# Kernel optimization log

Measured on AMD Instinct MI355X. Metric: run time of the kernel, lower is better.

Reference implementation:

```python
import jax, jax.numpy as jnp
import numpy as np

N, E, D, G, L = 100_000, 500_000, 128, 512, 4
BN_EPS = 1e-5

def _bn(v, g, b):
    # BatchNorm1d in training mode: biased batch stats over node/graph axis
    m = v.mean(0)
    var = v.var(0)
    return (v - m) * jax.lax.rsqrt(var + BN_EPS) * g + b

def setup_inputs() -> dict:
    key = jax.random.key(0)
    ks = jax.random.split(key, 12)
    s = 0.05
    return {
        "x": jax.random.normal(ks[0], (N, D), jnp.float32),
        "edge_index": jax.random.randint(ks[1], (2, E), 0, N, jnp.int64),
        "batch": jnp.sort(jax.random.randint(ks[2], (N,), 0, G, jnp.int64)),
        "num_graphs": G,
        "W1": jax.random.normal(ks[3], (L, D, 2 * D), jnp.float32) * s,
        "b1": jnp.zeros((L, 2 * D), jnp.float32),
        "g1": jnp.ones((L, 2 * D), jnp.float32),
        "be1": jnp.zeros((L, 2 * D), jnp.float32),
        "W2": jax.random.normal(ks[4], (L, 2 * D, D), jnp.float32) * s,
        "b2": jnp.zeros((L, D), jnp.float32),
        "gbn": jnp.ones((L, D), jnp.float32),
        "bbn": jnp.zeros((L, D), jnp.float32),
        "eps": jnp.zeros((L,), jnp.float32),
        "cW1": jax.random.normal(ks[5], (3 * D, D), jnp.float32) * s,
        "cb1": jnp.zeros((D,), jnp.float32),
        "cg": jnp.ones((D,), jnp.float32),
        "cbeta": jnp.zeros((D,), jnp.float32),
        "cW2": jax.random.normal(ks[6], (D, D // 2), jnp.float32) * s,
        "cb2": jnp.zeros((D // 2,), jnp.float32),
        "cW3": jax.random.normal(ks[7], (D // 2, 2), jnp.float32) * s,
        "cb3": jnp.zeros((2,), jnp.float32),
    }

def reference(x, edge_index, batch, num_graphs, W1, b1, g1, be1, W2, b2, gbn, bbn, eps,
              cW1, cb1, cg, cbeta, cW2, cb2, cW3, cb3):
    n = x.shape[0]
    src, dst = edge_index[0], edge_index[1]
    for l in range(W1.shape[0]):
        # GINConv: mlp((1+eps)*x + sum_{j in N(i)} x_j)  (scatter-add to dst)
        agg = jax.ops.segment_sum(x[src], dst, num_segments=n)
        h = (1.0 + eps[l]) * x + agg
        h = jax.nn.relu(_bn(h @ W1[l] + b1[l], g1[l], be1[l]))
        h = h @ W2[l] + b2[l]
        x = jax.nn.relu(_bn(h, gbn[l], bbn[l]))  # outer BN + ReLU (dropout off: eval)
    # multi-pool readout: add / mean / max per graph
    s = jax.ops.segment_sum(x, batch, num_segments=num_graphs)
    cnt = jax.ops.segment_sum(jnp.ones((n,), x.dtype), batch, num_segments=num_graphs)
    mean = s / jnp.maximum(cnt, 1.0)[:, None]
    mx = jax.ops.segment_max(x, batch, num_segments=num_graphs)
    z = jnp.concatenate([s, mean, mx], axis=-1)  # [G, 3*D]
    z = jax.nn.relu(_bn(z @ cW1 + cb1, cg, cbeta))
    z = jax.nn.relu(z @ cW2 + cb2)
    return z @ cW3 + cb3
```

## Files before the change

kernel.cpp:

```cpp
#include <hip/hip_runtime.h>
#include <cstdint>
#include <cstddef>

#define NN 100000
#define EE 500000
#define DD 128
#define GG 512
#define LL 4
#define BN_EPS 1e-5f

typedef __attribute__((ext_vector_type(8))) short short8;
typedef __attribute__((ext_vector_type(8))) unsigned short ushort8v;
typedef __attribute__((ext_vector_type(4))) float f32x4;

static __device__ __forceinline__ unsigned short f2bf(float f) {
  union { float f; unsigned u; } v;
  v.f = f;
  unsigned r = v.u + 0x7fffu + ((v.u >> 16) & 1u);
  return (unsigned short)(r >> 16);
}
static __device__ __forceinline__ float bf2f(unsigned short u) {
  union { unsigned u; float f; } v;
  v.u = ((unsigned)u) << 16;
  return v.f;
}


__global__ void k_hist(const int* __restrict__ ei, int* __restrict__ cnt) {
  int e = blockIdx.x * 256 + threadIdx.x;
  if (e < EE) {
    int d = ei[EE + e];
    if (d >= 0 && d < NN) atomicAdd(&cnt[d], 1);
  }
}

__global__ void k_part(const int* __restrict__ cnt, int* __restrict__ part) {
  __shared__ int sm[1024];
  int t = threadIdx.x;
  int i = blockIdx.x * 1024 + t;
  sm[t] = (i < NN) ? cnt[i] : 0;
  __syncthreads();
  for (int off = 512; off > 0; off >>= 1) {
    if (t < off) sm[t] += sm[t + off];
    __syncthreads();
  }
  if (t == 0) part[blockIdx.x] = sm[0];
}

__global__ void k_scanpart(const int* __restrict__ part, int* __restrict__ partx, int nb) {
  __shared__ int sm[128];
  int t = threadIdx.x;
  int v = (t < nb) ? part[t] : 0;
  sm[t] = v;
  __syncthreads();
  for (int off = 1; off < 128; off <<= 1) {
    int u = (t >= off) ? sm[t - off] : 0;
    __syncthreads();
    sm[t] += u;
    __syncthreads();
  }
  if (t < nb) partx[t] = sm[t] - v;
}

__global__ void k_rs(const int* __restrict__ cnt, const int* __restrict__ partx,
                     int* __restrict__ rs, int* __restrict__ cur) {
  __shared__ int sm[1024];
  int t = threadIdx.x;
  int i = blockIdx.x * 1024 + t;
  int v = (i < NN) ? cnt[i] : 0;
  sm[t] = v;
  __syncthreads();
  for (int off = 1; off < 1024; off <<= 1) {
    int u = (t >= off) ? sm[t - off] : 0;
    __syncthreads();
    sm[t] += u;
    __syncthreads();
  }
  if (i < NN) {
    int excl = partx[blockIdx.x] + sm[t] - v;
    rs[i] = excl;
    cur[i] = excl;
    if (i == NN - 1) rs[NN] = excl + v;
  }
}

__global__ void k_fill(const int* __restrict__ ei, int* __restrict__ cur,
                       int* __restrict__ ci) {
  int e = blockIdx.x * 256 + threadIdx.x;
  if (e < EE) {
    int s = ei[e];
    int d = ei[EE + e];
    if (d >= 0 && d < NN && s >= 0 && s < NN) {
      int pos = atomicAdd(&cur[d], 1);
      if (pos >= 0 && pos < EE) ci[pos] = s;
    }
  }
}


__global__ void k_conv(const float* __restrict__ W1, const float* __restrict__ W2,
                       unsigned short* __restrict__ W1t, unsigned short* __restrict__ W2t) {
  int idx = blockIdx.x * 256 + threadIdx.x;
  if (idx < 4 * 256 * 128) {
    {
      int l = idx >> 15, rem = idx & 32767;
      int nc = rem >> 7, k = rem & 127;
      W1t[idx] = f2bf(W1[(l << 15) + k * 256 + nc]);
    }
    {
      int l = idx >> 15, rem = idx & 32767;
      int nc = rem >> 8, k = rem & 255;
      W2t[idx] = f2bf(W2[(l << 15) + k * 128 + nc]);
    }
  }
}


__global__ void k_x2bf(const float* __restrict__ x, unsigned short* __restrict__ xb) {
  int i = blockIdx.x * 256 + threadIdx.x;
  if (i < NN * DD / 4) {
    float4 v = *(const float4*)(x + (size_t)i * 4);
    ushort4 o;
    o.x = f2bf(v.x); o.y = f2bf(v.y); o.z = f2bf(v.z); o.w = f2bf(v.w);
    *(ushort4*)(xb + (size_t)i * 4) = o;
  }
}


__global__ __launch_bounds__(256) void k_agg_bf16(
    const unsigned short* __restrict__ X, const int* __restrict__ rs,
    const int* __restrict__ ci, const float* __restrict__ epsv, int l, int mode,
    const float* __restrict__ tsc, const float* __restrict__ tsh,
    unsigned short* __restrict__ h0, int n) {
  int idx = blockIdx.x * 256 + threadIdx.x;
  int node = idx >> 4;
  int c8 = (idx & 15) << 3;
  if (node >= n) return;
  float sa[8], sb[8];
  if (mode) {
    float4 a0 = *(const float4*)(tsc + c8), a1 = *(const float4*)(tsc + c8 + 4);
    float4 b0 = *(const float4*)(tsh + c8), b1 = *(const float4*)(tsh + c8 + 4);
    sa[0] = a0.x; sa[1] = a0.y; sa[2] = a0.z; sa[3] = a0.w;
    sa[4] = a1.x; sa[5] = a1.y; sa[6] = a1.z; sa[7] = a1.w;
    sb[0] = b0.x; sb[1] = b0.y; sb[2] = b0.z; sb[3] = b0.w;
    sb[4] = b1.x; sb[5] = b1.y; sb[6] = b1.z; sb[7] = b1.w;
  }
  float se = 1.f + epsv[l];
  ushort8v v = *(const ushort8v*)(X + (size_t)node * DD + c8);
  float acc[8];
#pragma unroll
  for (int j = 0; j < 8; ++j) {
    float f = bf2f(v[j]);
    if (mode) f = fmaxf(0.f, f * sa[j] + sb[j]);
    acc[j] = se * f;
  }
  int e0 = rs[node], e1 = rs[node + 1];
  ushort8v un;
  if (e0 < e1) un = *(const ushort8v*)(X + (size_t)ci[e0] * DD + c8);
  for (int e = e0; e < e1; ++e) {
    ushort8v uc = un;
    if (e + 1 < e1) un = *(const ushort8v*)(X + (size_t)ci[e + 1] * DD + c8);
#pragma unroll
    for (int j = 0; j < 8; ++j) {
      float f = bf2f(uc[j]);
      if (mode) f = fmaxf(0.f, f * sa[j] + sb[j]);
      acc[j] += f;
    }
  }
  ushort8v o;
#pragma unroll
  for (int j = 0; j < 8; ++j) o[j] = f2bf(acc[j]);
  *(ushort8v*)(h0 + (size_t)node * DD + c8) = o;
}


template <int K, int NC>
__global__ __launch_bounds__(512) void k_gemm(
    const unsigned short* __restrict__ A, int mode, const float* __restrict__ tsc,
    const float* __restrict__ tsh, const unsigned short* __restrict__ Bt,
    const float* __restrict__ bias, unsigned short* __restrict__ C,
    float* __restrict__ psum, float* __restrict__ psq, int n) {
  constexpr int KC = 64;
  constexpr int KT = K / KC;
  constexpr int NT = NC / 128;
  constexpr int P = KT * NT;
  constexpr int AST = 72;
  constexpr int CTP = 136;
  __shared__ __align__(16) unsigned short smem[2 * 128 * AST];
  __shared__ float bsum[128], bsq[128];
  unsigned short* Asm = smem;
  unsigned short* Bsm = smem + 128 * AST;
  unsigned short* Ct = smem;

  int tid = threadIdx.x;
  int lane = tid & 63, wave = tid >> 6;
  int quad = lane >> 4, l15 = lane & 15;
  int row0 = blockIdx.x * 128;
  int blk = blockIdx.x;

  ushort8v pa[2], pb[2];
#pragma unroll
  for (int it = 0; it < 2; ++it) {
    int f = tid + it * 512;
    int r = f >> 3;
    int c8 = (f & 7) << 3;
    int gr = row0 + r;
    pa[it] = (ushort8v){0, 0, 0, 0, 0, 0, 0, 0};
    if (gr < n) pa[it] = *(const ushort8v*)(A + (size_t)gr * K + c8);
    pb[it] = *(const ushort8v*)(Bt + (size_t)r * K + c8);
  }

  f32x4 acc[8];
  for (int p = 0; p < P; ++p) {
    int cg = p / KT, kc = p % KT;
    if (kc == 0) {
#pragma unroll
      for (int j = 0; j < 8; ++j) acc[j] = (f32x4){0.f, 0.f, 0.f, 0.f};
    }
#pragma unroll
    for (int it = 0; it < 2; ++it) {
      int f = tid + it * 512;
      int r = f >> 3;
      int c8 = (f & 7) << 3;
      ushort8v v = pa[it];
      if (mode) {
        int kg = kc * KC + c8;
        float4 s0 = *(const float4*)(tsc + kg);
        float4 s1 = *(const float4*)(tsc + kg + 4);
        float4 t0 = *(const float4*)(tsh + kg);
        float4 t1 = *(const float4*)(tsh + kg + 4);
        float sa[8] = {s0.x, s0.y, s0.z, s0.w, s1.x, s1.y, s1.z, s1.w};
        float sb[8] = {t0.x, t0.y, t0.z, t0.w, t1.x, t1.y, t1.z, t1.w};
#pragma unroll
        for (int j = 0; j < 8; ++j)
          v[j] = f2bf(fmaxf(0.f, bf2f(v[j]) * sa[j] + sb[j]));
      }
      *(ushort8v*)(&Asm[r * AST + c8]) = v;
      *(ushort8v*)(&Bsm[r * AST + c8]) = pb[it];
    }
    __syncthreads();
    if (p + 1 < P) {
      int cg2 = (p + 1) / KT, kc2 = (p + 1) % KT;
#pragma unroll
      for (int it = 0; it < 2; ++it) {
        int f = tid + it * 512;
        int r = f >> 3;
        int c8 = (f & 7) << 3;
        int gr = row0 + r;
        pa[it] = (ushort8v){0, 0, 0, 0, 0, 0, 0, 0};
        if (gr < n) pa[it] = *(const ushort8v*)(A + (size_t)gr * K + kc2 * KC + c8);
        pb[it] = *(const ushort8v*)(Bt + (size_t)(cg2 * 128 + r) * K + kc2 * KC + c8);
      }
    }
#pragma unroll
    for (int kk = 0; kk < KC; kk += 32) {
      int ko = kk + quad * 8;
      short8 av = *(const short8*)(&Asm[(wave * 16 + l15) * AST + ko]);
#pragma unroll
      for (int cf = 0; cf < 8; ++cf) {
        short8 bv = *(const short8*)(&Bsm[(cf * 16 + l15) * AST + ko]);
        acc[cf] = __builtin_amdgcn_mfma_f32_16x16x32_bf16(av, bv, acc[cf], 0, 0, 0);
      }
    }
    if (kc == KT - 1) {
      __syncthreads();
      if (tid < 128) { bsum[tid] = 0.f; bsq[tid] = 0.f; }
      float s8[8], q8[8];
#pragma unroll
      for (int j = 0; j < 8; ++j) { s8[j] = 0.f; q8[j] = 0.f; }
      int lrbase = wave * 16 + quad * 4;
#pragma unroll
      for (int cf = 0; cf < 8; ++cf) {
        int col = cg * 128 + cf * 16 + l15;
        float bv = bias[col];
#pragma unroll
        for (int reg = 0; reg < 4; ++reg) {
          int lr = lrbase + reg;
          float e = acc[cf][reg] + bv;
          Ct[lr * CTP + cf * 16 + l15] = f2bf(e);
          if (row0 + lr < n) { s8[cf] += e; q8[cf] += e * e; }
        }
      }
#pragma unroll
      for (int cf = 0; cf < 8; ++cf) {
        s8[cf] += __shfl_xor(s8[cf], 16, 64);
        s8[cf] += __shfl_xor(s8[cf], 32, 64);
        q8[cf] += __shfl_xor(q8[cf], 16, 64);
        q8[cf] += __shfl_xor(q8[cf], 32, 64);
      }
      __syncthreads();
      if (quad == 0) {
#pragma unroll
        for (int cf = 0; cf < 8; ++cf) {
          atomicAdd(&bsum[cf * 16 + l15], s8[cf]);
          atomicAdd(&bsq[cf * 16 + l15], q8[cf]);
        }
      }
#pragma unroll
      for (int it = 0; it < 4; ++it) {
        int f = tid + it * 512;
        int r = f >> 4;
        int c8 = (f & 15) << 3;
        int gr = row0 + r;
        if (gr < n)
          *(ushort8v*)(C + (size_t)gr * NC + cg * 128 + c8) =
              *(const ushort8v*)(&Ct[r * CTP + c8]);
      }
      __syncthreads();
      if (tid < 128) {
        psum[(size_t)blk * NC + cg * 128 + tid] = bsum[tid];
        psq[(size_t)blk * NC + cg * 128 + tid] = bsq[tid];
      }
    } else {
      __syncthreads();
    }
  }
}


__global__ __launch_bounds__(256) void k_finred(
    const float* __restrict__ psum, const float* __restrict__ psq, int nb, int nc,
    const float* __restrict__ g, const float* __restrict__ be,
    float* __restrict__ osc, float* __restrict__ osh, float invn) {
  __shared__ float ws[4], wq[4];
  int col = blockIdx.x;
  int t = threadIdx.x;
  float s = 0.f, q = 0.f;
  for (int b = t; b < nb; b += 256) {
    s += psum[(size_t)b * nc + col];
    q += psq[(size_t)b * nc + col];
  }
#pragma unroll
  for (int off = 32; off > 0; off >>= 1) {
    s += __shfl_xor(s, off, 64);
    q += __shfl_xor(q, off, 64);
  }
  if ((t & 63) == 0) { ws[t >> 6] = s; wq[t >> 6] = q; }
  __syncthreads();
  if (t == 0) {
    s = ws[0] + ws[1] + ws[2] + ws[3];
    q = wq[0] + wq[1] + wq[2] + wq[3];
    float m = s * invn;
    float v = fmaxf(q * invn - m * m, 0.f);
    float sc = g[col] * rsqrtf(v + BN_EPS);
    osc[col] = sc;
    osh[col] = be[col] - m * sc;
  }
}


__global__ __launch_bounds__(256) void k_statz(
    const float* __restrict__ z1, const float* __restrict__ g,
    const float* __restrict__ be, float* __restrict__ osc, float* __restrict__ osh) {
  __shared__ float ws[4], wq[4];
  int col = blockIdx.x;
  int t = threadIdx.x;
  float s = 0.f, q = 0.f;
  for (int b = t; b < GG; b += 256) {
    float v = z1[(size_t)b * 128 + col];
    s += v;
    q += v * v;
  }
#pragma unroll
  for (int off = 32; off > 0; off >>= 1) {
    s += __shfl_xor(s, off, 64);
    q += __shfl_xor(q, off, 64);
  }
  if ((t & 63) == 0) { ws[t >> 6] = s; wq[t >> 6] = q; }
  __syncthreads();
  if (t == 0) {
    s = ws[0] + ws[1] + ws[2] + ws[3];
    q = wq[0] + wq[1] + wq[2] + wq[3];
    float m = s / (float)GG;
    float v = fmaxf(q / (float)GG - m * m, 0.f);
    float sc = g[col] * rsqrtf(v + BN_EPS);
    osc[col] = sc;
    osh[col] = be[col] - m * sc;
  }
}


static __device__ __forceinline__ int lb_i32(const int* a, int n, int key) {
  int lo = 0, hi = n;
  while (lo < hi) {
    int mid = (lo + hi) >> 1;
    if (a[mid] < key) lo = mid + 1; else hi = mid;
  }
  return lo;
}

__global__ __launch_bounds__(512) void k_pool(
    const unsigned short* __restrict__ X, const int* __restrict__ batch,
    const float* __restrict__ tsc, const float* __restrict__ tsh,
    float* __restrict__ z, int n) {
  __shared__ int slo, shi;
  __shared__ float ssum[8][128], smax[8][128];
  int g = blockIdx.x;
  int t = threadIdx.x;
  int sg = t >> 6;
  int c2 = (t & 63) << 1;
  if (t == 0) {
    slo = lb_i32(batch, n, g);
    shi = lb_i32(batch, n, g + 1);
  }
  __syncthreads();
  int lo = slo, hi = shi;
  float a0 = tsc[c2], a1 = tsc[c2 + 1];
  float b0 = tsh[c2], b1 = tsh[c2 + 1];
  float s0 = 0.f, s1 = 0.f;
  float m0 = -3.402823466e38f, m1 = -3.402823466e38f;
  for (int i = lo + sg; i < hi; i += 8) {
    unsigned u = *(const unsigned*)(X + (size_t)i * DD + c2);
    float v0 = fmaxf(0.f, bf2f((unsigned short)(u & 0xffff)) * a0 + b0);
    float v1 = fmaxf(0.f, bf2f((unsigned short)(u >> 16)) * a1 + b1);
    s0 += v0; m0 = fmaxf(m0, v0);
    s1 += v1; m1 = fmaxf(m1, v1);
  }
  ssum[sg][c2] = s0; ssum[sg][c2 + 1] = s1;
  smax[sg][c2] = m0; smax[sg][c2 + 1] = m1;
  __syncthreads();
  if (t < 128) {
    float S = 0.f, M = -3.402823466e38f;
#pragma unroll
    for (int k = 0; k < 8; ++k) {
      S += ssum[k][t];
      M = fmaxf(M, smax[k][t]);
    }
    float cntf = (float)(hi - lo);
    z[(size_t)g * 384 + t] = S;
    z[(size_t)g * 384 + 128 + t] = S / fmaxf(cntf, 1.f);
    z[(size_t)g * 384 + 256 + t] = M;
  }
}


__global__ void k_cls1(const float* __restrict__ z, const float* __restrict__ cW1,
                       const float* __restrict__ cb1, float* __restrict__ z1) {
  __shared__ float zr[384];
  int g = blockIdx.x;
  int c = threadIdx.x;
  for (int i = c; i < 384; i += 128) zr[i] = z[(size_t)g * 384 + i];
  __syncthreads();
  float s = cb1[c];
#pragma unroll 4
  for (int k = 0; k < 384; ++k) s = fmaf(zr[k], cW1[(size_t)k * 128 + c], s);
  z1[(size_t)g * 128 + c] = s;
}

__global__ void k_cls2(const float* __restrict__ z1, const float* __restrict__ csc,
                       const float* __restrict__ csh, const float* __restrict__ cW2,
                       const float* __restrict__ cb2, const float* __restrict__ cW3,
                       const float* __restrict__ cb3, float* __restrict__ out) {
  __shared__ float z1n[128];
  __shared__ float z2s[64];
  int g = blockIdx.x;
  int t = threadIdx.x;
  z1n[t] = fmaxf(0.f, z1[(size_t)g * 128 + t] * csc[t] + csh[t]);
  __syncthreads();
  if (t < 64) {
    float s = cb2[t];
#pragma unroll 4
    for (int k = 0; k < 128; ++k) s = fmaf(z1n[k], cW2[(size_t)k * 64 + t], s);
    z2s[t] = fmaxf(0.f, s);
  }
  __syncthreads();
  if (t < 2) {
    float s = cb3[t];
#pragma unroll 4
    for (int c = 0; c < 64; ++c) s = fmaf(z2s[c], cW3[(size_t)c * 2 + t], s);
    out[(size_t)g * 2 + t] = s;
  }
}


extern "C" void kernel_launch(void* const* d_in, const int* in_sizes, int n_in,
                              void* d_out, int out_size, void* d_ws, size_t ws_size,
                              hipStream_t stream) {
  const float* x = (const float*)d_in[0];
  const int* ei = (const int*)d_in[1];
  const int* batch = (const int*)d_in[2];
  const float* W1 = (const float*)d_in[4];
  const float* b1 = (const float*)d_in[5];
  const float* g1 = (const float*)d_in[6];
  const float* be1 = (const float*)d_in[7];
  const float* W2 = (const float*)d_in[8];
  const float* b2 = (const float*)d_in[9];
  const float* gbn = (const float*)d_in[10];
  const float* bbn = (const float*)d_in[11];
  const float* epsv = (const float*)d_in[12];
  const float* cW1 = (const float*)d_in[13];
  const float* cb1 = (const float*)d_in[14];
  const float* cg = (const float*)d_in[15];
  const float* cbeta = (const float*)d_in[16];
  const float* cW2 = (const float*)d_in[17];
  const float* cb2 = (const float*)d_in[18];
  const float* cW3 = (const float*)d_in[19];
  const float* cb3 = (const float*)d_in[20];
  float* out = (float*)d_out;

  char* p = (char*)d_ws;
  auto alloc = [&](size_t bytes) {
    char* r = p;
    p += (bytes + 255) & ~(size_t)255;
    return r;
  };
  const int NB = (NN + 127) / 128;
  int* cnt = (int*)alloc((size_t)NN * 4);
  int* rs = (int*)alloc((size_t)(NN + 1) * 4);
  int* cur = (int*)alloc((size_t)NN * 4);
  int* ci = (int*)alloc((size_t)EE * 4);
  int* part = (int*)alloc(128 * 4);
  int* partx = (int*)alloc(128 * 4);
  unsigned short* xbf = (unsigned short*)alloc((size_t)NN * DD * 2);
  unsigned short* h0 = (unsigned short*)alloc((size_t)NN * DD * 2);
  unsigned short* h1 = (unsigned short*)alloc((size_t)NN * 2 * DD * 2);
  unsigned short* xp = (unsigned short*)alloc((size_t)NN * DD * 2);
  float* psum = (float*)alloc((size_t)NB * 256 * 4);
  float* psq = (float*)alloc((size_t)NB * 256 * 4);
  float* tsc1 = (float*)alloc(256 * 4);
  float* tsh1 = (float*)alloc(256 * 4);
  float* tscX = (float*)alloc(128 * 4);
  float* tshX = (float*)alloc(128 * 4);
  float* zbuf = (float*)alloc((size_t)GG * 384 * 4);
  float* z1 = (float*)alloc((size_t)GG * 128 * 4);
  unsigned short* W1t = (unsigned short*)alloc((size_t)4 * 256 * 128 * 2);
  unsigned short* W2t = (unsigned short*)alloc((size_t)4 * 128 * 256 * 2);
  (void)ws_size; (void)n_in; (void)in_sizes; (void)out_size;

  k_conv<<<512, 256, 0, stream>>>(W1, W2, W1t, W2t);
  k_x2bf<<<(NN * DD / 4 + 255) / 256, 256, 0, stream>>>(x, xbf);

  hipMemsetAsync(cnt, 0, (size_t)NN * 4, stream);
  k_hist<<<(EE + 255) / 256, 256, 0, stream>>>(ei, cnt);
  const int nscan = (NN + 1023) / 1024;
  k_part<<<nscan, 1024, 0, stream>>>(cnt, part);
  k_scanpart<<<1, 128, 0, stream>>>(part, partx, nscan);
  k_rs<<<nscan, 1024, 0, stream>>>(cnt, partx, rs, cur);
  k_fill<<<(EE + 255) / 256, 256, 0, stream>>>(ei, cur, ci);

  for (int l = 0; l < LL; ++l) {
    const unsigned short* Xl = (l == 0) ? xbf : xp;
    k_agg_bf16<<<(NN * 16 + 255) / 256, 256, 0, stream>>>(
        Xl, rs, ci, epsv, l, (l > 0) ? 1 : 0, tscX, tshX, h0, NN);
    k_gemm<128, 256><<<NB, 512, 0, stream>>>(
        h0, 0, nullptr, nullptr, W1t + (size_t)l * 256 * 128,
        b1 + (size_t)l * 256, h1, psum, psq, NN);
    k_finred<<<256, 256, 0, stream>>>(psum, psq, NB, 256, g1 + (size_t)l * 256,
                                      be1 + (size_t)l * 256, tsc1, tsh1, 1.0f / NN);
    k_gemm<256, 128><<<NB, 512, 0, stream>>>(
        h1, 1, tsc1, tsh1, W2t + (size_t)l * 128 * 256,
        b2 + (size_t)l * 128, xp, psum, psq, NN);
    k_finred<<<128, 256, 0, stream>>>(psum, psq, NB, 128, gbn + (size_t)l * 128,
                                      bbn + (size_t)l * 128, tscX, tshX, 1.0f / NN);
  }

  k_pool<<<GG, 512, 0, stream>>>(xp, batch, tscX, tshX, zbuf, NN);
  k_cls1<<<GG, 128, 0, stream>>>(zbuf, cW1, cb1, z1);
  k_statz<<<128, 256, 0, stream>>>(z1, cg, cbeta, tscX, tshX);
  k_cls2<<<GG, 128, 0, stream>>>(z1, tscX, tshX, cW2, cb2, cW3, cb3, out);
}
```

Baseline: 765.7 us.

## Keep A fragments in registers and stage full weight matrix in LDS for GEMM

Rewrites the fused GEMM+BN-stats kernel so each wave loads its 16-row A slice straight into registers for the full K, stages the whole transposed weight matrix in LDS once, and computes all output columns in one pass with swapped MFMA operands. The per-K-chunk LDS staging of A and the associated barriers go away, and output is written directly from registers without an LDS transpose. Column statistics are reduced with lane shuffles plus a per-wave LDS buffer. In exchange it holds many accumulators and A registers (CF up to 16 f32x4, KT up to 8 short8), which raises register pressure, and the weight tile occupies a large LDS footprint (up to 256x136 shorts ≈ 68KB), while the launch bound now requests 4 blocks per CU.

```diff
diff --git a/kernel.cpp b/kernel.cpp
--- a/kernel.cpp
+++ b/kernel.cpp
@@ -175,145 +175,113 @@
 
 
 template <int K, int NC>
-__global__ __launch_bounds__(512) void k_gemm(
+__global__ __launch_bounds__(512, 4) void k_gemm(
     const unsigned short* __restrict__ A, int mode, const float* __restrict__ tsc,
     const float* __restrict__ tsh, const unsigned short* __restrict__ Bt,
     const float* __restrict__ bias, unsigned short* __restrict__ C,
     float* __restrict__ psum, float* __restrict__ psq, int n) {
-  constexpr int KC = 64;
-  constexpr int KT = K / KC;
-  constexpr int NT = NC / 128;
-  constexpr int P = KT * NT;
-  constexpr int AST = 72;
-  constexpr int CTP = 136;
-  __shared__ __align__(16) unsigned short smem[2 * 128 * AST];
-  __shared__ float bsum[128], bsq[128];
-  unsigned short* Asm = smem;
-  unsigned short* Bsm = smem + 128 * AST;
-  unsigned short* Ct = smem;
+  constexpr int KT = K / 32;
+  constexpr int CF = NC / 16;
+  constexpr int BP = K + 8;
+  constexpr int CH = K / 8;
+  __shared__ __align__(16) unsigned short Bsm[NC * BP];
 
   int tid = threadIdx.x;
   int lane = tid & 63, wave = tid >> 6;
   int quad = lane >> 4, l15 = lane & 15;
-  int row0 = blockIdx.x * 128;
-  int blk = blockIdx.x;
-
-  ushort8v pa[2], pb[2];
-#pragma unroll
-  for (int it = 0; it < 2; ++it) {
+  int r = blockIdx.x * 128 + wave * 16 + l15;
+  bool valid = r < n;
+
+  short8 av[KT];
+#pragma unroll
+  for (int ks = 0; ks < KT; ++ks) {
+    av[ks] = (short8){0, 0, 0, 0, 0, 0, 0, 0};
+    if (valid) av[ks] = *(const short8*)(A + (size_t)r * K + ks * 32 + quad * 8);
+  }
+
+#pragma unroll
+  for (int it = 0; it < NC * CH / 512; ++it) {
     int f = tid + it * 512;
-    int r = f >> 3;
-    int c8 = (f & 7) << 3;
-    int gr = row0 + r;
-    pa[it] = (ushort8v){0, 0, 0, 0, 0, 0, 0, 0};
-    if (gr < n) pa[it] = *(const ushort8v*)(A + (size_t)gr * K + c8);
-    pb[it] = *(const ushort8v*)(Bt + (size_t)r * K + c8);
-  }
-
-  f32x4 acc[8];
-  for (int p = 0; p < P; ++p) {
-    int cg = p / KT, kc = p % KT;
-    if (kc == 0) {
-#pragma unroll
-      for (int j = 0; j < 8; ++j) acc[j] = (f32x4){0.f, 0.f, 0.f, 0.f};
-    }
-#pragma unroll
-    for (int it = 0; it < 2; ++it) {
-      int f = tid + it * 512;
-      int r = f >> 3;
-      int c8 = (f & 7) << 3;
-      ushort8v v = pa[it];
-      if (mode) {
-        int kg = kc * KC + c8;
-        float4 s0 = *(const float4*)(tsc + kg);
-        float4 s1 = *(const float4*)(tsc + kg + 4);
-        float4 t0 = *(const float4*)(tsh + kg);
-        float4 t1 = *(const float4*)(tsh + kg + 4);
-        float sa[8] = {s0.x, s0.y, s0.z, s0.w, s1.x, s1.y, s1.z, s1.w};
-        float sb[8] = {t0.x, t0.y, t0.z, t0.w, t1.x, t1.y, t1.z, t1.w};
-#pragma unroll
-        for (int j = 0; j < 8; ++j)
-          v[j] = f2bf(fmaxf(0.f, bf2f(v[j]) * sa[j] + sb[j]));
-      }
-      *(ushort8v*)(&Asm[r * AST + c8]) = v;
-      *(ushort8v*)(&Bsm[r * AST + c8]) = pb[it];
-    }
-    __syncthreads();
-    if (p + 1 < P) {
-      int cg2 = (p + 1) / KT, kc2 = (p + 1) % KT;
-#pragma unroll
-      for (int it = 0; it < 2; ++it) {
-        int f = tid + it * 512;
-        int r = f >> 3;
-        int c8 = (f & 7) << 3;
-        int gr = row0 + r;
-        pa[it] = (ushort8v){0, 0, 0, 0, 0, 0, 0, 0};
-        if (gr < n) pa[it] = *(const ushort8v*)(A + (size_t)gr * K + kc2 * KC + c8);
-        pb[it] = *(const ushort8v*)(Bt + (size_t)(cg2 * 128 + r) * K + kc2 * KC + c8);
-      }
-    }
-#pragma unroll
-    for (int kk = 0; kk < KC; kk += 32) {
-      int ko = kk + quad * 8;
-      short8 av = *(const short8*)(&Asm[(wave * 16 + l15) * AST + ko]);
-#pragma unroll
-      for (int cf = 0; cf < 8; ++cf) {
-        short8 bv = *(const short8*)(&Bsm[(cf * 16 + l15) * AST + ko]);
-        acc[cf] = __builtin_amdgcn_mfma_f32_16x16x32_bf16(av, bv, acc[cf], 0, 0, 0);
-      }
-    }
-    if (kc == KT - 1) {
-      __syncthreads();
-      if (tid < 128) { bsum[tid] = 0.f; bsq[tid] = 0.f; }
-      float s8[8], q8[8];
-#pragma unroll
-      for (int j = 0; j < 8; ++j) { s8[j] = 0.f; q8[j] = 0.f; }
-      int lrbase = wave * 16 + quad * 4;
-#pragma unroll
-      for (int cf = 0; cf < 8; ++cf) {
-        int col = cg * 128 + cf * 16 + l15;
-        float bv = bias[col];
-#pragma unroll
-        for (int reg = 0; reg < 4; ++reg) {
-          int lr = lrbase + reg;
-          float e = acc[cf][reg] + bv;
-          Ct[lr * CTP + cf * 16 + l15] = f2bf(e);
-          if (row0 + lr < n) { s8[cf] += e; q8[cf] += e * e; }
-        }
-      }
-#pragma unroll
-      for (int cf = 0; cf < 8; ++cf) {
-        s8[cf] += __shfl_xor(s8[cf], 16, 64);
-        s8[cf] += __shfl_xor(s8[cf], 32, 64);
-        q8[cf] += __shfl_xor(q8[cf], 16, 64);
-        q8[cf] += __shfl_xor(q8[cf], 32, 64);
-      }
-      __syncthreads();
-      if (quad == 0) {
-#pragma unroll
-        for (int cf = 0; cf < 8; ++cf) {
-          atomicAdd(&bsum[cf * 16 + l15], s8[cf]);
-          atomicAdd(&bsq[cf * 16 + l15], q8[cf]);
-        }
-      }
-#pragma unroll
-      for (int it = 0; it < 4; ++it) {
-        int f = tid + it * 512;
-        int r = f >> 4;
-        int c8 = (f & 15) << 3;
-        int gr = row0 + r;
-        if (gr < n)
-          *(ushort8v*)(C + (size_t)gr * NC + cg * 128 + c8) =
-              *(const ushort8v*)(&Ct[r * CTP + c8]);
-      }
-      __syncthreads();
-      if (tid < 128) {
-        psum[(size_t)blk * NC + cg * 128 + tid] = bsum[tid];
-        psq[(size_t)blk * NC + cg * 128 + tid] = bsq[tid];
-      }
-    } else {
-      __syncthreads();
-    }
+    int br = f / CH;
+    int c8 = (f % CH) * 8;
+    *(ushort8v*)(&Bsm[br * BP + c8]) = *(const ushort8v*)(Bt + (size_t)br * K + c8);
+  }
+
+  if (mode) {
+#pragma unroll
+    for (int ks = 0; ks < KT; ++ks) {
+      int kg = ks * 32 + quad * 8;
+      float4 s0 = *(const float4*)(tsc + kg), s1 = *(const float4*)(tsc + kg + 4);
+      float4 t0 = *(const float4*)(tsh + kg), t1 = *(const float4*)(tsh + kg + 4);
+      float sa[8] = {s0.x, s0.y, s0.z, s0.w, s1.x, s1.y, s1.z, s1.w};
+      float sb[8] = {t0.x, t0.y, t0.z, t0.w, t1.x, t1.y, t1.z, t1.w};
+      short8 v = av[ks];
+#pragma unroll
+      for (int j = 0; j < 8; ++j)
+        v[j] = (short)f2bf(fmaxf(0.f, bf2f((unsigned short)v[j]) * sa[j] + sb[j]));
+      av[ks] = v;
+    }
+  }
+
+  __syncthreads();
+
+  f32x4 acc[CF];
+#pragma unroll
+  for (int cf = 0; cf < CF; ++cf) acc[cf] = (f32x4){0.f, 0.f, 0.f, 0.f};
+
+#pragma unroll
+  for (int ks = 0; ks < KT; ++ks) {
+#pragma unroll
+    for (int cf = 0; cf < CF; ++cf) {
+      short8 bv = *(const short8*)(&Bsm[(cf * 16 + l15) * BP + ks * 32 + quad * 8]);
+      acc[cf] = __builtin_amdgcn_mfma_f32_16x16x32_bf16(bv, av[ks], acc[cf], 0, 0, 0);
+    }
+  }
+
+  __syncthreads();
+
+  float* Ssum = (float*)Bsm;
+  float* Ssq = Ssum + 8 * NC;
+
+#pragma unroll
+  for (int cf = 0; cf < CF; ++cf) {
+    float4 bb = *(const float4*)(bias + cf * 16 + quad * 4);
+    float e0 = acc[cf][0] + bb.x;
+    float e1 = acc[cf][1] + bb.y;
+    float e2 = acc[cf][2] + bb.z;
+    float e3 = acc[cf][3] + bb.w;
+    if (valid) {
+      ushort4 o;
+      o.x = f2bf(e0); o.y = f2bf(e1); o.z = f2bf(e2); o.w = f2bf(e3);
+      *(ushort4*)(C + (size_t)r * NC + cf * 16 + quad * 4) = o;
+    }
+    float s0 = valid ? e0 : 0.f, s1 = valid ? e1 : 0.f;
+    float s2 = valid ? e2 : 0.f, s3 = valid ? e3 : 0.f;
+    float q0 = s0 * e0, q1 = s1 * e1, q2 = s2 * e2, q3 = s3 * e3;
+#pragma unroll
+    for (int m = 1; m < 16; m <<= 1) {
+      s0 += __shfl_xor(s0, m, 64); s1 += __shfl_xor(s1, m, 64);
+      s2 += __shfl_xor(s2, m, 64); s3 += __shfl_xor(s3, m, 64);
+      q0 += __shfl_xor(q0, m, 64); q1 += __shfl_xor(q1, m, 64);
+      q2 += __shfl_xor(q2, m, 64); q3 += __shfl_xor(q3, m, 64);
+    }
+    if (l15 == 0) {
+      *(float4*)(&Ssum[wave * NC + cf * 16 + quad * 4]) = (float4){s0, s1, s2, s3};
+      *(float4*)(&Ssq[wave * NC + cf * 16 + quad * 4]) = (float4){q0, q1, q2, q3};
+    }
+  }
+
+  __syncthreads();
+
+  if (tid < NC) {
+    float s = 0.f, q = 0.f;
+#pragma unroll
+    for (int w = 0; w < 8; ++w) {
+      s += Ssum[w * NC + tid];
+      q += Ssq[w * NC + tid];
+    }
+    psum[(size_t)blockIdx.x * NC + tid] = s;
+    psq[(size_t)blockIdx.x * NC + tid] = q;
   }
 }
 
```

Measured after the change: 862.7 us. 1.13x slower.

## Derive first BN stats from input moments and fuse both MLP GEMMs

Applied to the files above, without the earlier changes.

The first BatchNorm's batch statistics are now computed algebraically from the second-moment matrix h0ᵀh0 and column sums of the GEMM input, projected through W1 (the b1 bias cancels under BN). This removes the need to materialize the 256-wide hidden activation before its stats are known. Both GEMMs then run in one fused kernel that keeps the hidden tile in shared memory, so the large h1 round trip to global memory is gone. In exchange there is an extra moment kernel with global atomics and more shared memory per block. Computing variance as E[x²]-mean² in fp32 from bf16 inputs may lose precision.

```diff
diff --git a/kernel.cpp b/kernel.cpp
--- a/kernel.cpp
+++ b/kernel.cpp
@@ -174,147 +174,283 @@
 }
 
 
-template <int K, int NC>
-__global__ __launch_bounds__(512) void k_gemm(
-    const unsigned short* __restrict__ A, int mode, const float* __restrict__ tsc,
-    const float* __restrict__ tsh, const unsigned short* __restrict__ Bt,
-    const float* __restrict__ bias, unsigned short* __restrict__ C,
-    float* __restrict__ psum, float* __restrict__ psq, int n) {
-  constexpr int KC = 64;
-  constexpr int KT = K / KC;
-  constexpr int NT = NC / 128;
-  constexpr int P = KT * NT;
+__global__ __launch_bounds__(512) void k_mom(
+    const unsigned short* __restrict__ h0, float* __restrict__ M2s,
+    float* __restrict__ css, int n) {
+  constexpr int HT = 264;
+  __shared__ __align__(16) unsigned short Ht[128 * HT];
+  __shared__ float lcs[128];
+  int tid = threadIdx.x;
+  int lane = tid & 63, wave = tid >> 6;
+  int quad = lane >> 4, l15 = lane & 15;
+  int n0 = blockIdx.x * 256;
+  if (tid < 128) lcs[tid] = 0.f;
+  int c8 = (tid & 15) << 3;
+  int rloc = tid >> 4;
+  float csr[8];
+#pragma unroll
+  for (int j = 0; j < 8; ++j) csr[j] = 0.f;
+  __syncthreads();
+#pragma unroll
+  for (int pass = 0; pass < 8; ++pass) {
+    int nl = rloc + pass * 32;
+    int gr = n0 + nl;
+    ushort8v v = (ushort8v){0, 0, 0, 0, 0, 0, 0, 0};
+    if (gr < n) v = *(const ushort8v*)(h0 + (size_t)gr * DD + c8);
+#pragma unroll
+    for (int j = 0; j < 8; ++j) {
+      Ht[(c8 + j) * HT + nl] = v[j];
+      csr[j] += bf2f(v[j]);
+    }
+  }
+#pragma unroll
+  for (int j = 0; j < 8; ++j) atomicAdd(&lcs[c8 + j], csr[j]);
+  __syncthreads();
+  f32x4 acc[8];
+#pragma unroll
+  for (int j = 0; j < 8; ++j) acc[j] = (f32x4){0.f, 0.f, 0.f, 0.f};
+#pragma unroll
+  for (int kc = 0; kc < 8; ++kc) {
+    int ko = kc * 32 + quad * 8;
+    short8 av = *(const short8*)(&Ht[(wave * 16 + l15) * HT + ko]);
+#pragma unroll
+    for (int j = 0; j < 8; ++j) {
+      short8 bv = *(const short8*)(&Ht[(j * 16 + l15) * HT + ko]);
+      acc[j] = __builtin_amdgcn_mfma_f32_16x16x32_bf16(av, bv, acc[j], 0, 0, 0);
+    }
+  }
+  int slab = blockIdx.x & 7;
+  float* M2 = M2s + (size_t)slab * (128 * 128);
+  int lr = wave * 16 + quad * 4;
+#pragma unroll
+  for (int j = 0; j < 8; ++j)
+#pragma unroll
+    for (int reg = 0; reg < 4; ++reg)
+      atomicAdd(&M2[(lr + reg) * 128 + j * 16 + l15], acc[j][reg]);
+  if (tid < 128) atomicAdd(&css[slab * 128 + tid], lcs[tid]);
+}
+
+__global__ void k_red(const float* __restrict__ M2s, const float* __restrict__ css,
+                      float* __restrict__ M2f, float* __restrict__ csf) {
+  int i = blockIdx.x * 256 + threadIdx.x;
+  float s = 0.f;
+#pragma unroll
+  for (int k = 0; k < 8; ++k) s += M2s[(size_t)k * 16384 + i];
+  M2f[i] = s;
+  if (i < 128) {
+    float c = 0.f;
+#pragma unroll
+    for (int k = 0; k < 8; ++k) c += css[k * 128 + i];
+    csf[i] = c;
+  }
+}
+
+__global__ __launch_bounds__(128) void k_bn1(
+    const float* __restrict__ M2, const float* __restrict__ cs,
+    const unsigned short* __restrict__ W1t_l, const float* __restrict__ g1_l,
+    const float* __restrict__ be1_l, float* __restrict__ osc,
+    float* __restrict__ osh) {
+  __shared__ float wsh[128];
+  __shared__ float red1[2], red2[2];
+  int c = blockIdx.x, t = threadIdx.x;
+  float w = bf2f(W1t_l[c * 128 + t]);
+  wsh[t] = w;
+  __syncthreads();
+  float inner = 0.f;
+#pragma unroll 4
+  for (int k = 0; k < 128; ++k) inner = fmaf(M2[t * 128 + k], wsh[k], inner);
+  float s1 = w * inner;
+  float s2 = w * cs[t];
+#pragma unroll
+  for (int off = 32; off > 0; off >>= 1) {
+    s1 += __shfl_xor(s1, off, 64);
+    s2 += __shfl_xor(s2, off, 64);
+  }
+  if ((t & 63) == 0) { red1[t >> 6] = s1; red2[t >> 6] = s2; }
+  __syncthreads();
+  if (t == 0) {
+    float q = (red1[0] + red1[1]) * (1.0f / NN);
+    float um = (red2[0] + red2[1]) * (1.0f / NN);
+    float var = fmaxf(q - um * um, 0.f);
+    float sc = g1_l[c] * rsqrtf(var + BN_EPS);
+    osc[c] = sc;
+    osh[c] = be1_l[c] - um * sc;
+  }
+}
+
+
+__global__ __launch_bounds__(512, 4) void k_gfused(
+    const unsigned short* __restrict__ A, const float* __restrict__ sc1,
+    const float* __restrict__ sh1, const unsigned short* __restrict__ W1t_l,
+    const unsigned short* __restrict__ W2t_l, const float* __restrict__ b2_l,
+    unsigned short* __restrict__ C, float* __restrict__ psum,
+    float* __restrict__ psq, int n) {
   constexpr int AST = 72;
-  constexpr int CTP = 136;
+  constexpr int HP = 136;
   __shared__ __align__(16) unsigned short smem[2 * 128 * AST];
+  __shared__ __align__(16) unsigned short H[128 * HP];
   __shared__ float bsum[128], bsq[128];
   unsigned short* Asm = smem;
   unsigned short* Bsm = smem + 128 * AST;
-  unsigned short* Ct = smem;
 
   int tid = threadIdx.x;
   int lane = tid & 63, wave = tid >> 6;
   int quad = lane >> 4, l15 = lane & 15;
   int row0 = blockIdx.x * 128;
-  int blk = blockIdx.x;
 
   ushort8v pa[2], pb[2];
-#pragma unroll
-  for (int it = 0; it < 2; ++it) {
+  f32x4 acc1[8], acc2[8];
+#pragma unroll
+  for (int j = 0; j < 8; ++j) acc2[j] = (f32x4){0.f, 0.f, 0.f, 0.f};
+
+#define LOADS1(cg, kc)                                                         \
+  {                                                                            \
+    _Pragma("unroll") for (int it = 0; it < 2; ++it) {                         \
+      int f = tid + it * 512, rr = f >> 3, c8 = (f & 7) << 3;                  \
+      int gr = row0 + rr;                                                      \
+      pa[it] = (ushort8v){0, 0, 0, 0, 0, 0, 0, 0};                             \
+      if (gr < n)                                                              \
+        pa[it] = *(const ushort8v*)(A + (size_t)gr * 128 + (kc)*64 + c8);      \
+      pb[it] = *(const ushort8v*)(W1t_l +                                      \
+                                  (size_t)((cg)*128 + rr) * 128 + (kc)*64 + c8); \
+    }                                                                          \
+  }
+#define LOADS2(kc2)                                                            \
+  {                                                                            \
+    _Pragma("unroll") for (int it = 0; it < 2; ++it) {                         \
+      int f = tid + it * 512, rr = f >> 3, c8 = (f & 7) << 3;                  \
+      pb[it] = *(const ushort8v*)(W2t_l + (size_t)rr * 256 + (kc2)*64 + c8);   \
+    }                                                                          \
+  }
+#define WRITES1                                                                \
+  {                                                                            \
+    _Pragma("unroll") for (int it = 0; it < 2; ++it) {                         \
+      int f = tid + it * 512, rr = f >> 3, c8 = (f & 7) << 3;                  \
+      *(ushort8v*)(&Asm[rr * AST + c8]) = pa[it];                              \
+      *(ushort8v*)(&Bsm[rr * AST + c8]) = pb[it];                              \
+    }                                                                          \
+  }
+#define WRITES2                                                                \
+  {                                                                            \
+    _Pragma("unroll") for (int it = 0; it < 2; ++it) {                         \
+      int f = tid + it * 512, rr = f >> 3, c8 = (f & 7) << 3;                  \
+      *(ushort8v*)(&Bsm[rr * AST + c8]) = pb[it];                              \
+    }                                                                          \
+  }
+#define ZERO1                                                                  \
+  {                                                                            \
+    _Pragma("unroll") for (int j = 0; j < 8; ++j)                              \
+        acc1[j] = (f32x4){0.f, 0.f, 0.f, 0.f};                                 \
+  }
+#define MFMAS1                                                                 \
+  {                                                                            \
+    _Pragma("unroll") for (int kk = 0; kk < 64; kk += 32) {                    \
+      int ko = kk + quad * 8;                                                  \
+      short8 av = *(const short8*)(&Asm[(wave * 16 + l15) * AST + ko]);        \
+      _Pragma("unroll") for (int cf = 0; cf < 8; ++cf) {                       \
+        short8 bv = *(const short8*)(&Bsm[(cf * 16 + l15) * AST + ko]);        \
+        acc1[cf] =                                                             \
+            __builtin_amdgcn_mfma_f32_16x16x32_bf16(av, bv, acc1[cf], 0, 0, 0); \
+      }                                                                        \
+    }                                                                          \
+  }
+#define MFMAS2(half)                                                           \
+  {                                                                            \
+    _Pragma("unroll") for (int kk = 0; kk < 64; kk += 32) {                    \
+      int ko = kk + quad * 8;                                                  \
+      short8 av =                                                              \
+          *(const short8*)(&H[(wave * 16 + l15) * HP + (half)*64 + ko]);       \
+      _Pragma("unroll") for (int cf = 0; cf < 8; ++cf) {                       \
+        short8 bv = *(const short8*)(&Bsm[(cf * 16 + l15) * AST + ko]);        \
+        acc2[cf] =                                                             \
+            __builtin_amdgcn_mfma_f32_16x16x32_bf16(av, bv, acc2[cf], 0, 0, 0); \
+      }                                                                        \
+    }                                                                          \
+  }
+#define EPI1(cg)                                                               \
+  {                                                                            \
+    int lrb = wave * 16 + quad * 4;                                            \
+    _Pragma("unroll") for (int cf = 0; cf < 8; ++cf) {                         \
+      int col = (cg)*128 + cf * 16 + l15;                                      \
+      float sc = sc1[col], sh = sh1[col];                                      \
+      _Pragma("unroll") for (int reg = 0; reg < 4; ++reg)                      \
+          H[(lrb + reg) * HP + cf * 16 + l15] =                                \
+              f2bf(fmaxf(0.f, acc1[cf][reg] * sc + sh));                       \
+    }                                                                          \
+  }
+
+  LOADS1(0, 0)
+  WRITES1 __syncthreads();
+  LOADS1(0, 1) ZERO1 MFMAS1 __syncthreads();
+  WRITES1 __syncthreads();
+  LOADS2(0) MFMAS1 EPI1(0) __syncthreads();
+  WRITES2 __syncthreads();
+  LOADS2(1) MFMAS2(0) __syncthreads();
+  WRITES2 __syncthreads();
+  LOADS1(1, 0) MFMAS2(1) __syncthreads();
+  WRITES1 __syncthreads();
+  LOADS1(1, 1) ZERO1 MFMAS1 __syncthreads();
+  WRITES1 __syncthreads();
+  LOADS2(2) MFMAS1 EPI1(1) __syncthreads();
+  WRITES2 __syncthreads();
+  LOADS2(3) MFMAS2(0) __syncthreads();
+  WRITES2 __syncthreads();
+  MFMAS2(1)
+
+  __syncthreads();
+  unsigned short* Ct = smem;
+  if (tid < 128) { bsum[tid] = 0.f; bsq[tid] = 0.f; }
+  float s8[8], q8[8];
+#pragma unroll
+  for (int j = 0; j < 8; ++j) { s8[j] = 0.f; q8[j] = 0.f; }
+  int lrbase = wave * 16 + quad * 4;
+#pragma unroll
+  for (int cf = 0; cf < 8; ++cf) {
+    float bv = b2_l[cf * 16 + l15];
+#pragma unroll
+    for (int reg = 0; reg < 4; ++reg) {
+      int lr = lrbase + reg;
+      float e = acc2[cf][reg] + bv;
+      Ct[lr * HP + cf * 16 + l15] = f2bf(e);
+      if (row0 + lr < n) { s8[cf] += e; q8[cf] += e * e; }
+    }
+  }
+#pragma unroll
+  for (int cf = 0; cf < 8; ++cf) {
+    s8[cf] += __shfl_xor(s8[cf], 16, 64);
+    s8[cf] += __shfl_xor(s8[cf], 32, 64);
+    q8[cf] += __shfl_xor(q8[cf], 16, 64);
+    q8[cf] += __shfl_xor(q8[cf], 32, 64);
+  }
+  __syncthreads();
+  if (quad == 0) {
+#pragma unroll
+    for (int cf = 0; cf < 8; ++cf) {
+      atomicAdd(&bsum[cf * 16 + l15], s8[cf]);
+      atomicAdd(&bsq[cf * 16 + l15], q8[cf]);
+    }
+  }
+#pragma unroll
+  for (int it = 0; it < 4; ++it) {
     int f = tid + it * 512;
-    int r = f >> 3;
-    int c8 = (f & 7) << 3;
+    int r = f >> 4, c8 = (f & 15) << 3;
     int gr = row0 + r;
-    pa[it] = (ushort8v){0, 0, 0, 0, 0, 0, 0, 0};
-    if (gr < n) pa[it] = *(const ushort8v*)(A + (size_t)gr * K + c8);
-    pb[it] = *(const ushort8v*)(Bt + (size_t)r * K + c8);
-  }
-
-  f32x4 acc[8];
-  for (int p = 0; p < P; ++p) {
-    int cg = p / KT, kc = p % KT;
-    if (kc == 0) {
-#pragma unroll
-      for (int j = 0; j < 8; ++j) acc[j] = (f32x4){0.f, 0.f, 0.f, 0.f};
-    }
-#pragma unroll
-    for (int it = 0; it < 2; ++it) {
-      int f = tid + it * 512;
-      int r = f >> 3;
-      int c8 = (f & 7) << 3;
-      ushort8v v = pa[it];
-      if (mode) {
-        int kg = kc * KC + c8;
-        float4 s0 = *(const float4*)(tsc + kg);
-        float4 s1 = *(const float4*)(tsc + kg + 4);
-        float4 t0 = *(const float4*)(tsh + kg);
-        float4 t1 = *(const float4*)(tsh + kg + 4);
-        float sa[8] = {s0.x, s0.y, s0.z, s0.w, s1.x, s1.y, s1.z, s1.w};
-        float sb[8] = {t0.x, t0.y, t0.z, t0.w, t1.x, t1.y, t1.z, t1.w};
-#pragma unroll
-        for (int j = 0; j < 8; ++j)
-          v[j] = f2bf(fmaxf(0.f, bf2f(v[j]) * sa[j] + sb[j]));
-      }
-      *(ushort8v*)(&Asm[r * AST + c8]) = v;
-      *(ushort8v*)(&Bsm[r * AST + c8]) = pb[it];
-    }
-    __syncthreads();
-    if (p + 1 < P) {
-      int cg2 = (p + 1) / KT, kc2 = (p + 1) % KT;
-#pragma unroll
-      for (int it = 0; it < 2; ++it) {
-        int f = tid + it * 512;
-        int r = f >> 3;
-        int c8 = (f & 7) << 3;
-        int gr = row0 + r;
-        pa[it] = (ushort8v){0, 0, 0, 0, 0, 0, 0, 0};
-        if (gr < n) pa[it] = *(const ushort8v*)(A + (size_t)gr * K + kc2 * KC + c8);
-        pb[it] = *(const ushort8v*)(Bt + (size_t)(cg2 * 128 + r) * K + kc2 * KC + c8);
-      }
-    }
-#pragma unroll
-    for (int kk = 0; kk < KC; kk += 32) {
-      int ko = kk + quad * 8;
-      short8 av = *(const short8*)(&Asm[(wave * 16 + l15) * AST + ko]);
-#pragma unroll
-      for (int cf = 0; cf < 8; ++cf) {
-        short8 bv = *(const short8*)(&Bsm[(cf * 16 + l15) * AST + ko]);
-        acc[cf] = __builtin_amdgcn_mfma_f32_16x16x32_bf16(av, bv, acc[cf], 0, 0, 0);
-      }
-    }
-    if (kc == KT - 1) {
-      __syncthreads();
-      if (tid < 128) { bsum[tid] = 0.f; bsq[tid] = 0.f; }
-      float s8[8], q8[8];
-#pragma unroll
-      for (int j = 0; j < 8; ++j) { s8[j] = 0.f; q8[j] = 0.f; }
-      int lrbase = wave * 16 + quad * 4;
-#pragma unroll
-      for (int cf = 0; cf < 8; ++cf) {
-        int col = cg * 128 + cf * 16 + l15;
-        float bv = bias[col];
-#pragma unroll
-        for (int reg = 0; reg < 4; ++reg) {
-          int lr = lrbase + reg;
-          float e = acc[cf][reg] + bv;
-          Ct[lr * CTP + cf * 16 + l15] = f2bf(e);
-          if (row0 + lr < n) { s8[cf] += e; q8[cf] += e * e; }
-        }
-      }
-#pragma unroll
-      for (int cf = 0; cf < 8; ++cf) {
-        s8[cf] += __shfl_xor(s8[cf], 16, 64);
-        s8[cf] += __shfl_xor(s8[cf], 32, 64);
-        q8[cf] += __shfl_xor(q8[cf], 16, 64);
-        q8[cf] += __shfl_xor(q8[cf], 32, 64);
-      }
-      __syncthreads();
-      if (quad == 0) {
-#pragma unroll
-        for (int cf = 0; cf < 8; ++cf) {
-          atomicAdd(&bsum[cf * 16 + l15], s8[cf]);
-          atomicAdd(&bsq[cf * 16 + l15], q8[cf]);
-        }
-      }
-#pragma unroll
-      for (int it = 0; it < 4; ++it) {
-        int f = tid + it * 512;
-        int r = f >> 4;
-        int c8 = (f & 15) << 3;
-        int gr = row0 + r;
-        if (gr < n)
-          *(ushort8v*)(C + (size_t)gr * NC + cg * 128 + c8) =
-              *(const ushort8v*)(&Ct[r * CTP + c8]);
-      }
-      __syncthreads();
-      if (tid < 128) {
-        psum[(size_t)blk * NC + cg * 128 + tid] = bsum[tid];
-        psq[(size_t)blk * NC + cg * 128 + tid] = bsq[tid];
-      }
-    } else {
-      __syncthreads();
-    }
-  }
+    if (gr < n)
+      *(ushort8v*)(C + (size_t)gr * 128 + c8) = *(const ushort8v*)(&Ct[r * HP + c8]);
+  }
+  __syncthreads();
+  if (tid < 128) {
+    psum[(size_t)blockIdx.x * 128 + tid] = bsum[tid];
+    psq[(size_t)blockIdx.x * 128 + tid] = bsq[tid];
+  }
+#undef LOADS1
+#undef LOADS2
+#undef WRITES1
+#undef WRITES2
+#undef ZERO1
+#undef MFMAS1
+#undef MFMAS2
+#undef EPI1
 }
 
 
@@ -497,6 +633,7 @@
   const float* cW3 = (const float*)d_in[19];
   const float* cb3 = (const float*)d_in[20];
   float* out = (float*)d_out;
+  (void)b1;
 
   char* p = (char*)d_ws;
   auto alloc = [&](size_t bytes) {
@@ -505,6 +642,7 @@
     return r;
   };
   const int NB = (NN + 127) / 128;
+  const int NMOM = (NN + 255) / 256;
   int* cnt = (int*)alloc((size_t)NN * 4);
   int* rs = (int*)alloc((size_t)(NN + 1) * 4);
   int* cur = (int*)alloc((size_t)NN * 4);
@@ -513,10 +651,9 @@
   int* partx = (int*)alloc(128 * 4);
   unsigned short* xbf = (unsigned short*)alloc((size_t)NN * DD * 2);
   unsigned short* h0 = (unsigned short*)alloc((size_t)NN * DD * 2);
-  unsigned short* h1 = (unsigned short*)alloc((size_t)NN * 2 * DD * 2);
   unsigned short* xp = (unsigned short*)alloc((size_t)NN * DD * 2);
-  float* psum = (float*)alloc((size_t)NB * 256 * 4);
-  float* psq = (float*)alloc((size_t)NB * 256 * 4);
+  float* psum = (float*)alloc((size_t)NB * 128 * 4);
+  float* psq = (float*)alloc((size_t)NB * 128 * 4);
   float* tsc1 = (float*)alloc(256 * 4);
   float* tsh1 = (float*)alloc(256 * 4);
   float* tscX = (float*)alloc(128 * 4);
@@ -525,6 +662,11 @@
   float* z1 = (float*)alloc((size_t)GG * 128 * 4);
   unsigned short* W1t = (unsigned short*)alloc((size_t)4 * 256 * 128 * 2);
   unsigned short* W2t = (unsigned short*)alloc((size_t)4 * 128 * 256 * 2);
+  float* mz = (float*)alloc((size_t)(8 * 128 * 128 + 8 * 128) * 4);
+  float* M2s = mz;
+  float* css = mz + 8 * 128 * 128;
+  float* M2f = (float*)alloc((size_t)128 * 128 * 4);
+  float* csf = (float*)alloc(128 * 4);
   (void)ws_size; (void)n_in; (void)in_sizes; (void)out_size;
 
   k_conv<<<512, 256, 0, stream>>>(W1, W2, W1t, W2t);
@@ -542,13 +684,14 @@
     const unsigned short* Xl = (l == 0) ? xbf : xp;
     k_agg_bf16<<<(NN * 16 + 255) / 256, 256, 0, stream>>>(
         Xl, rs, ci, epsv, l, (l > 0) ? 1 : 0, tscX, tshX, h0, NN);
-    k_gemm<128, 256><<<NB, 512, 0, stream>>>(
-        h0, 0, nullptr, nullptr, W1t + (size_t)l * 256 * 128,
-        b1 + (size_t)l * 256, h1, psum, psq, NN);
-    k_finred<<<256, 256, 0, stream>>>(psum, psq, NB, 256, g1 + (size_t)l * 256,
-                                      be1 + (size_t)l * 256, tsc1, tsh1, 1.0f / NN);
-    k_gemm<256, 128><<<NB, 512, 0, stream>>>(
-        h1, 1, tsc1, tsh1, W2t + (size_t)l * 128 * 256,
+    hipMemsetAsync(mz, 0, (size_t)(8 * 128 * 128 + 8 * 128) * 4, stream);
+    k_mom<<<NMOM, 512, 0, stream>>>(h0, M2s, css, NN);
+    k_red<<<64, 256, 0, stream>>>(M2s, css, M2f, csf);
+    k_bn1<<<256, 128, 0, stream>>>(M2f, csf, W1t + (size_t)l * 256 * 128,
+                                   g1 + (size_t)l * 256, be1 + (size_t)l * 256,
+                                   tsc1, tsh1);
+    k_gfused<<<NB, 512, 0, stream>>>(
+        h0, tsc1, tsh1, W1t + (size_t)l * 256 * 128, W2t + (size_t)l * 128 * 256,
         b2 + (size_t)l * 128, xp, psum, psq, NN);
     k_finred<<<128, 256, 0, stream>>>(psum, psq, NB, 128, gbn + (size_t)l * 128,
                                       bbn + (size_t)l * 128, tscX, tshX, 1.0f / NN);
```

Measured after the change: 825.8 us. +7.9%, slower.
